# Kernel tuning notes

Hardware: AMD Instinct MI355X
Metric: run time of the kernel (lower is better)

Reference implementation:

```python
import jax, jax.numpy as jnp
import numpy as np
from jax import lax

NH = 4          # num_head
DIM = 512       # attention dim
VDIM = 512      # v_dim
QDIM = 1024     # q_dim
KS = 100        # loc_kernel_size -> conv width 2*KS+1
KN = 100        # loc_kernel_num
TEMP = 0.5      # temperature
BS, TS = 8, 2048


def setup_inputs() -> dict:
    key = jax.random.key(0)
    ks = jax.random.split(key, 12)
    s = 0.05
    return {
        "dec_state": jax.random.normal(ks[0], (BS, QDIM), jnp.float32),
        "enc_feat": jax.random.normal(ks[1], (BS, TS, VDIM), jnp.float32),
        "enc_len": jax.random.randint(ks[2], (BS,), TS // 2, TS + 1).astype(jnp.int32),
        "Wq": jax.random.normal(ks[3], (NH * DIM, QDIM), jnp.float32) * s,
        "bq": jnp.zeros((NH * DIM,), jnp.float32),
        "Wk": jax.random.normal(ks[4], (NH * DIM, VDIM), jnp.float32) * s,
        "bk": jnp.zeros((NH * DIM,), jnp.float32),
        "Wv": jax.random.normal(ks[5], (NH * VDIM, VDIM), jnp.float32) * s,
        "bv": jnp.zeros((NH * VDIM,), jnp.float32),
        "loc_conv_w": jax.random.normal(ks[6], (KN, NH, 2 * KS + 1), jnp.float32) * s,
        "loc_proj_w": jax.random.normal(ks[7], (DIM, KN), jnp.float32) * s,
        "gen_w": jax.random.normal(ks[8], (1, DIM), jnp.float32) * s,
        "gen_b": jnp.zeros((1,), jnp.float32),
        "merge_w": jax.random.normal(ks[9], (VDIM, NH * VDIM), jnp.float32) * s,
        "merge_b": jnp.zeros((VDIM,), jnp.float32),
    }


def reference(dec_state, enc_feat, enc_len, Wq, bq, Wk, bk, Wv, bv,
              loc_conv_w, loc_proj_w, gen_w, gen_b, merge_w, merge_b):
    bs, ts, _ = enc_feat.shape
    # query: [bs, nh, dim]
    query = jnp.tanh(dec_state @ Wq.T + bq).reshape(bs, NH, DIM)
    # key/value: [bs, nh, ts, dim]/[bs, nh, ts, v_dim]
    key = jnp.tanh(enc_feat @ Wk.T + bk).reshape(bs, ts, NH, DIM).transpose(0, 2, 1, 3)
    value = jnp.tanh(enc_feat @ Wv.T + bv).reshape(bs, ts, NH, VDIM).transpose(0, 2, 1, 3)
    # mask & initial (uniform-over-valid) previous attention
    pos = jnp.arange(ts)
    pad_mask = pos[None, :] >= enc_len[:, None]                      # [bs, ts] True = padded
    prev = jnp.where(pad_mask, 0.0, 1.0 / enc_len[:, None].astype(jnp.float32))  # [bs, ts]
    prev_att = jnp.broadcast_to(prev[:, None, :], (bs, NH, ts))      # [bs, nh, ts]
    # location features: Conv1d(nh -> kn, width 2*KS+1, pad KS, no bias)
    conv = lax.conv_general_dilated(prev_att, loc_conv_w, (1,), [(KS, KS)],
                                    dimension_numbers=("NCH", "OIH", "NCH"))  # [bs, kn, ts]
    loc = jnp.tanh(jnp.einsum("bkt,dk->btd", conv, loc_proj_w))      # [bs, ts, dim]
    # additive energy: gen_energy(tanh(k + q + loc))
    e = jnp.tanh(key + query[:, :, None, :] + loc[:, None, :, :])    # [bs, nh, ts, dim]
    energy = jnp.einsum("bhtd,d->bht", e, gen_w[0]) + gen_b[0]
    energy = energy / TEMP
    energy = jnp.where(pad_mask[:, None, :], -jnp.inf, energy)
    attn = jax.nn.softmax(energy, axis=-1)                           # [bs, nh, ts]
    ctx = jnp.einsum("bht,bhtv->bhv", attn, value).reshape(bs, NH * VDIM)
    context = ctx @ merge_w.T + merge_b                              # [bs, v_dim]
    return attn, context
```

## Files before the change

### kernel.cpp

```cpp
#include <hip/hip_runtime.h>
#include <math.h>

#define NH 4
#define DIM 512
#define VDIM 512
#define QDIM 1024
#define KS 100
#define KN 100
#define TEMPERATURE 0.5f
#define BS 8
#define TS 2048
#define NHD (NH * DIM)

#define WS_QUERY   0
#define WS_QTAB    16384
#define WS_ENERGYP 119808
#define WS_CTX     381952
#define WS_P       398336
#define WS_F32_END 418536

typedef __bf16 bf16x8 __attribute__((ext_vector_type(8)));
typedef __bf16 bf16x4 __attribute__((ext_vector_type(4)));
typedef _Float16 f16x8 __attribute__((ext_vector_type(8)));
typedef float  f32x4  __attribute__((ext_vector_type(4)));

#define AS1(p) ((const __attribute__((address_space(1))) void*)(p))
#define AS3(p) ((__attribute__((address_space(3))) void*)(p))

__device__ __forceinline__ float fast_tanh(float x) {
    float e = __expf(2.0f * x);
    return 1.0f - __fdividef(2.0f, e + 1.0f);
}

#define NE4 (BS * TS * VDIM / 4)
#define NW4 (NHD * VDIM / 4)
#define NCVT ((NE4 + 2 * NW4) / 256)
#define NQ2  (NHD / 4)
__global__ void k_pre(const float* __restrict__ enc, const float* __restrict__ Wk,
                      const float* __restrict__ Wv, __bf16* __restrict__ enc_bf,
                      __bf16* __restrict__ wk_bf, __bf16* __restrict__ wv_bf,
                      const float* __restrict__ dec, const float* __restrict__ Wq,
                      const float* __restrict__ bq, float* __restrict__ query,
                      const float* __restrict__ convw, float* __restrict__ P) {
    const int bx = blockIdx.x;
    if (bx < NCVT) {
        int i = bx * blockDim.x + threadIdx.x;
        const float* src; __bf16* dst; int k;
        if (i < NE4)            { src = enc; dst = enc_bf; k = i; }
        else if (i < NE4 + NW4) { src = Wk;  dst = wk_bf;  k = i - NE4; }
        else                    { src = Wv;  dst = wv_bf;  k = i - NE4 - NW4; }
        float4 v = ((const float4*)src)[k];
        bf16x4 o;
        o[0] = (__bf16)v.x; o[1] = (__bf16)v.y; o[2] = (__bf16)v.z; o[3] = (__bf16)v.w;
        ((bf16x4*)dst)[k] = o;
    } else if (bx < NCVT + NQ2) {
        int o = (bx - NCVT) * 4 + (threadIdx.x >> 6);
        int lane = threadIdx.x & 63;
        const float* wr = Wq + (size_t)o * QDIM;
        float s[BS];
        #pragma unroll
        for (int b = 0; b < BS; ++b) s[b] = 0.f;
        #pragma unroll
        for (int i = 0; i < QDIM / 64; ++i) {
            float wv = wr[lane + 64 * i];
            #pragma unroll
            for (int b = 0; b < BS; ++b)
                s[b] = fmaf(wv, dec[b * QDIM + lane + 64 * i], s[b]);
        }
        #pragma unroll
        for (int off = 32; off > 0; off >>= 1)
            #pragma unroll
            for (int b = 0; b < BS; ++b) s[b] += __shfl_down(s[b], off);
        if (lane == 0) {
            float bias = bq[o];
            #pragma unroll
            for (int b = 0; b < BS; ++b) query[b * NHD + o] = tanhf(s[b] + bias);
        }
    } else {
        __shared__ float cs[KN * (2 * KS + 1)];
        int tid = threadIdx.x;
        for (int i = tid; i < KN * (2 * KS + 1); i += 256) {
            int k = i / (2 * KS + 1);
            int dt = i - k * (2 * KS + 1);
            const float* wr = convw + k * (NH * (2 * KS + 1)) + dt;
            cs[i] = wr[0] + wr[201] + wr[402] + wr[603];
        }
        __syncthreads();
        if (tid < KN) {
            float acc = 0.f;
            P[tid] = 0.f;
            const float* c = cs + tid * (2 * KS + 1);
            for (int dt = 0; dt < 2 * KS + 1; ++dt) {
                acc += c[dt];
                P[(dt + 1) * KN + tid] = acc;
            }
        }
    }
}

__global__ void k_qtab(const float* __restrict__ P, const float* __restrict__ projw,
                       float* __restrict__ Qtab, float* __restrict__ ctx) {
    int tid = threadIdx.x;
    if (blockIdx.x >= 2 * KS + 2) {
        int z = (blockIdx.x - (2 * KS + 2)) * 512 + tid;
        ((float4*)ctx)[z] = make_float4(0.f, 0.f, 0.f, 0.f);
        return;
    }
    int j = blockIdx.x;
    __shared__ float Pc[KN];
    if (tid < KN) Pc[tid] = P[j * KN + tid];
    __syncthreads();
    const float* pr = projw + tid * KN;
    float s = 0.f;
    #pragma unroll 4
    for (int k = 0; k < KN; ++k) s = fmaf(pr[k], Pc[k], s);
    Qtab[j * DIM + tid] = s;
}

__global__ __launch_bounds__(512, 4) void k_fused(
    const __bf16* __restrict__ enc_bf, const __bf16* __restrict__ wk_bf,
    const __bf16* __restrict__ wv_bf, const float* __restrict__ bk,
    const float* __restrict__ bv, const float* __restrict__ gen_w,
    const int* __restrict__ enc_len, const float* __restrict__ query,
    const float* __restrict__ Qtab, float* __restrict__ energyP,
    _Float16* __restrict__ val) {
    const int bid = blockIdx.x;
    const int b   = bid >> 8;
    const int t0  = ((bid >> 4) & 15) << 7;
    const int n0  = ((((bid >> 3) & 1) << 3) | (bid & 7)) << 7;
    const int len = enc_len[b];
    if (t0 >= len) return;
    const int tid = threadIdx.x;
    const int w = tid >> 6, lane = tid & 63;
    const int wy = w >> 2, wx = w & 3;
    const int col = lane & 15, quad = lane >> 4;
    __shared__ __bf16 smem[3 * 12288];
    f32x4 accE[4][2], accV[4][2];
    #pragma unroll
    for (int i = 0; i < 4; ++i)
        #pragma unroll
        for (int j = 0; j < 2; ++j) { accE[i][j] = (f32x4)0.f; accV[i][j] = (f32x4)0.f; }
    const int sm = tid >> 2;
    const int sj = (tid & 3) ^ (sm & 3) ^ ((sm >> 2) & 3);
    const __bf16* gpA  = enc_bf + ((size_t)b * TS + t0) * VDIM + (size_t)sm * VDIM + sj * 8;
    const __bf16* gpBk = wk_bf + ((size_t)n0 + sm) * VDIM + sj * 8;
    const __bf16* gpBv = wv_bf + ((size_t)n0 + sm) * VDIM + sj * 8;
    const int cfr = quad ^ (col & 3) ^ ((col >> 2) & 3);
    const char* pbase = (const char*)smem;
    const int offA = (((wy * 64 + col) * 4 + cfr) << 4);
    const int offB = (((wx * 32 + col) * 4 + cfr) << 4);
    #define STG(sbe)                                                               \
        __builtin_amdgcn_global_load_lds(AS1(gpA),  AS3(smem + (sbe) + w * 512), 16, 0, 0);        \
        __builtin_amdgcn_global_load_lds(AS1(gpBk), AS3(smem + (sbe) + 4096 + w * 512), 16, 0, 0); \
        __builtin_amdgcn_global_load_lds(AS1(gpBv), AS3(smem + (sbe) + 8192 + w * 512), 16, 0, 0); \
        gpA += 32; gpBk += 32; gpBv += 32;
    STG(0)
    STG(12288)
    #pragma unroll
    for (int kk = 0; kk < 16; ++kk) {
        if (kk < 15)
            asm volatile("s_waitcnt vmcnt(3) lgkmcnt(0)\n\ts_barrier" ::: "memory");
        else
            asm volatile("s_waitcnt vmcnt(0) lgkmcnt(0)\n\ts_barrier" ::: "memory");
        if (kk < 14) {
            const int sbe = ((kk + 2) % 3) * 12288;
            STG(sbe)
        }
        const int bo = (kk % 3) * 24576;
        bf16x8 af[4], bfr[2];
        #pragma unroll
        for (int i = 0; i < 4; ++i) af[i] = *(const bf16x8*)(pbase + bo + offA + i * 1024);
        #pragma unroll
        for (int j = 0; j < 2; ++j) bfr[j] = *(const bf16x8*)(pbase + bo + 8192 + offB + j * 1024);
        #pragma unroll
        for (int i = 0; i < 4; ++i)
            #pragma unroll
            for (int j = 0; j < 2; ++j)
                accE[i][j] = __builtin_amdgcn_mfma_f32_16x16x32_bf16(af[i], bfr[j], accE[i][j], 0, 0, 0);
        #pragma unroll
        for (int j = 0; j < 2; ++j) bfr[j] = *(const bf16x8*)(pbase + bo + 16384 + offB + j * 1024);
        #pragma unroll
        for (int i = 0; i < 4; ++i)
            #pragma unroll
            for (int j = 0; j < 2; ++j)
                accV[i][j] = __builtin_amdgcn_mfma_f32_16x16x32_bf16(af[i], bfr[j], accV[i][j], 0, 0, 0);
    }
    #undef STG
    __syncthreads();

    _Float16* stage = (_Float16*)smem;
    float* red = (float*)((char*)smem + 32768);

    const int h = n0 >> 9;
    const float inv_len = 1.0f / (float)len;
    float qv[2], gw[2], bkv[2], bvv[2], lI[2];
    int dj[2];
    #pragma unroll
    for (int j = 0; j < 2; ++j) {
        int n = n0 + wx * 32 + j * 16 + col;
        dj[j] = n & (DIM - 1);
        qv[j] = query[b * NHD + n];
        gw[j] = gen_w[dj[j]];
        bkv[j] = bk[n];
        bvv[j] = bv[n];
        lI[j] = fast_tanh((Qtab[(2 * KS + 1) * DIM + dj[j]] - Qtab[dj[j]]) * inv_len);
    }
    #pragma unroll
    for (int i = 0; i < 4; ++i) {
        #pragma unroll
        for (int r = 0; r < 4; ++r) {
            int tl = wy * 64 + i * 16 + quad * 4 + r;
            int t = t0 + tl;
            float l[2];
            if (t >= KS && t < len - KS) {
                #pragma unroll
                for (int j = 0; j < 2; ++j) l[j] = lI[j];
            } else {
                int lo = KS - t; if (lo < 0) lo = 0;
                int hi = KS - t + len - 1; if (hi > 2 * KS) hi = 2 * KS;
                bool has = (hi >= lo);
                #pragma unroll
                for (int j = 0; j < 2; ++j) {
                    float cv = has
                        ? (Qtab[(hi + 1) * DIM + dj[j]] - Qtab[lo * DIM + dj[j]]) * inv_len
                        : 0.f;
                    l[j] = fast_tanh(cv);
                }
            }
            float s = 0.f;
            #pragma unroll
            for (int j = 0; j < 2; ++j) {
                float key = fast_tanh(accE[i][j][r] + bkv[j]);
                float e = fast_tanh(key + qv[j] + l[j]);
                s = fmaf(e, gw[j], s);
            }
            s += __shfl_xor(s, 1); s += __shfl_xor(s, 2);
            s += __shfl_xor(s, 4); s += __shfl_xor(s, 8);
            if (col == 0) red[tl * 4 + wx] = s;
        }
    }
    #pragma unroll
    for (int j = 0; j < 2; ++j) {
        #pragma unroll
        for (int i = 0; i < 4; ++i)
            #pragma unroll
            for (int r = 0; r < 4; ++r) {
                int tl = wy * 64 + i * 16 + quad * 4 + r;
                stage[tl * 128 + wx * 32 + j * 16 + col] =
                    (_Float16)fast_tanh(accV[i][j][r] + bvv[j]);
            }
    }
    __syncthreads();
    if (tid < 128) {
        float s = red[tid * 4] + red[tid * 4 + 1] + red[tid * 4 + 2] + red[tid * 4 + 3];
        energyP[(size_t)((n0 >> 7) & 3) * 65536 + (size_t)(b * NH + h) * TS + t0 + tid] = s;
    }
    #pragma unroll
    for (int it = 0; it < 4; ++it) {
        int idx = it * 512 + tid;
        int row = idx >> 4, seg = idx & 15;
        *(float4*)((char*)(val + ((size_t)b * TS + t0 + row) * NHD + n0) + seg * 16) =
            ((const float4*)stage)[idx];
    }
}

__global__ void k_softmax(const float* __restrict__ energyP, const int* __restrict__ enc_len,
                          const float* __restrict__ gen_b, float* __restrict__ attn) {
    int bh = blockIdx.x;
    int b = bh >> 2;
    int len = enc_len[b];
    int tid = threadIdx.x;
    int w = tid >> 6, lane = tid & 63;
    const float gb = gen_b[0];
    const float* e0 = energyP + (size_t)bh * TS;
    float ev[4];
    float mx = -INFINITY;
    #pragma unroll
    for (int i = 0; i < 4; ++i) {
        int t = i * 512 + tid;
        float e = -INFINITY;
        if (t < len) {
            float s = e0[t] + e0[65536 + t] + e0[131072 + t] + e0[196608 + t];
            e = (s + gb) * (1.0f / TEMPERATURE);
        }
        ev[i] = e;
        mx = fmaxf(mx, e);
    }
    __shared__ float sred[8], ssum[8];
    #pragma unroll
    for (int off = 32; off > 0; off >>= 1) mx = fmaxf(mx, __shfl_xor(mx, off));
    if (lane == 0) sred[w] = mx;
    __syncthreads();
    #pragma unroll
    for (int k = 0; k < 8; ++k) mx = fmaxf(mx, sred[k]);
    float ls = 0.f;
    #pragma unroll
    for (int i = 0; i < 4; ++i) {
        float ex = __expf(ev[i] - mx);
        ev[i] = ex;
        ls += ex;
    }
    #pragma unroll
    for (int off = 32; off > 0; off >>= 1) ls += __shfl_xor(ls, off);
    if (lane == 0) ssum[w] = ls;
    __syncthreads();
    float tot = 0.f;
    #pragma unroll
    for (int k = 0; k < 8; ++k) tot += ssum[k];
    float inv = 1.0f / tot;
    #pragma unroll
    for (int i = 0; i < 4; ++i)
        attn[(size_t)bh * TS + i * 512 + tid] = ev[i] * inv;
}

__global__ __launch_bounds__(256) void k_ctx2(const _Float16* __restrict__ val,
                                              const float* __restrict__ attn,
                                              const int* __restrict__ enc_len,
                                              float* __restrict__ ctx) {
    const int blk = blockIdx.x;
    const int b   = blk >> 7;
    const int nc  = (blk >> 3) & 15;
    const int tsl = blk & 7;
    const int len = enc_len[b];
    const int t0  = tsl * 256;
    if (t0 >= len) return;
    const int n0 = nc * 128;
    const int h  = n0 >> 9;
    const int tid = threadIdx.x;
    const int tn = tid & 15, tr = tid >> 4;
    const float* ar = attn + (size_t)(b * NH + h) * TS;
    float acc[8];
    #pragma unroll
    for (int k = 0; k < 8; ++k) acc[k] = 0.f;
    int tend = t0 + 256; if (tend > len) tend = len;
    for (int t = t0 + tr; t < tend; t += 16) {
        float a = ar[t];
        f16x8 v = *(const f16x8*)(val + ((size_t)b * TS + t) * NHD + n0 + tn * 8);
        #pragma unroll
        for (int k = 0; k < 8; ++k) acc[k] = fmaf(a, (float)v[k], acc[k]);
    }
    __shared__ float cred[16][128];
    #pragma unroll
    for (int k = 0; k < 8; ++k) cred[tr][tn * 8 + k] = acc[k];
    __syncthreads();
    if (tid < 128) {
        float s = 0.f;
        #pragma unroll
        for (int r = 0; r < 16; ++r) s += cred[r][tid];
        atomicAdd(&ctx[(size_t)b * NHD + n0 + tid], s);
    }
}

__global__ void k_merge(const float* __restrict__ ctx, const float* __restrict__ mw,
                        const float* __restrict__ mb, float* __restrict__ out) {
    int o = blockIdx.x * 4 + (threadIdx.x >> 6);
    int lane = threadIdx.x & 63;
    const float* wr = mw + (size_t)o * NHD;
    float s[BS];
    #pragma unroll
    for (int b = 0; b < BS; ++b) s[b] = 0.f;
    #pragma unroll
    for (int i = 0; i < NHD / 64; ++i) {
        float wv = wr[lane + 64 * i];
        #pragma unroll
        for (int b = 0; b < BS; ++b)
            s[b] = fmaf(wv, ctx[b * NHD + lane + 64 * i], s[b]);
    }
    #pragma unroll
    for (int off = 32; off > 0; off >>= 1)
        #pragma unroll
        for (int b = 0; b < BS; ++b) s[b] += __shfl_down(s[b], off);
    if (lane == 0) {
        float bias = mb[o];
        #pragma unroll
        for (int b = 0; b < BS; ++b) out[b * VDIM + o] = s[b] + bias;
    }
}

extern "C" void kernel_launch(void* const* d_in, const int* in_sizes, int n_in,
                              void* d_out, int out_size, void* d_ws, size_t ws_size,
                              hipStream_t stream) {
    const float* dec     = (const float*)d_in[0];
    const float* enc     = (const float*)d_in[1];
    const int*   enc_len = (const int*)d_in[2];
    const float* Wq      = (const float*)d_in[3];
    const float* bq      = (const float*)d_in[4];
    const float* Wk      = (const float*)d_in[5];
    const float* bk      = (const float*)d_in[6];
    const float* Wv      = (const float*)d_in[7];
    const float* bv      = (const float*)d_in[8];
    const float* convw   = (const float*)d_in[9];
    const float* projw   = (const float*)d_in[10];
    const float* gen_w   = (const float*)d_in[11];
    const float* gen_b   = (const float*)d_in[12];
    const float* merge_w = (const float*)d_in[13];
    const float* merge_b = (const float*)d_in[14];

    float* out    = (float*)d_out;
    float* ws     = (float*)d_ws;
    float* query  = ws + WS_QUERY;
    float* Qtab   = ws + WS_QTAB;
    float* energyP= ws + WS_ENERGYP;
    float* ctx    = ws + WS_CTX;
    float* Pws    = ws + WS_P;
    __bf16* enc_bf = (__bf16*)((char*)d_ws + (size_t)WS_F32_END * 4);
    __bf16* wk_bf  = enc_bf + (size_t)BS * TS * VDIM;
    __bf16* wv_bf  = wk_bf + (size_t)NHD * VDIM;
    _Float16* val  = (_Float16*)(wv_bf + (size_t)NHD * VDIM);

    k_pre<<<dim3(NCVT + NQ2 + 1), dim3(256), 0, stream>>>(
        enc, Wk, Wv, enc_bf, wk_bf, wv_bf, dec, Wq, bq, query, convw, Pws);
    k_qtab<<<dim3(2 * KS + 2 + 8), dim3(512), 0, stream>>>(Pws, projw, Qtab, ctx);
    k_fused<<<dim3(2048), dim3(512), 0, stream>>>(
        enc_bf, wk_bf, wv_bf, bk, bv, gen_w, enc_len, query, Qtab, energyP, val);
    k_softmax<<<dim3(BS * NH), dim3(512), 0, stream>>>(energyP, enc_len, gen_b, out);
    k_ctx2<<<dim3(BS * 16 * 8), dim3(256), 0, stream>>>(val, out, enc_len, ctx);
    k_merge<<<dim3(VDIM / 4), dim3(256), 0, stream>>>(ctx, merge_w, merge_b, out + 65536);
}
```

Baseline: 287.7 us.

## Enlarge fused GEMM tile to 256x128 with swizzled staging and MFMA priority

```diff
diff --git a/kernel.cpp b/kernel.cpp
--- a/kernel.cpp
+++ b/kernel.cpp
@@ -117,7 +117,7 @@
     Qtab[j * DIM + tid] = s;
 }
 
-__global__ __launch_bounds__(512, 4) void k_fused(
+__global__ __launch_bounds__(512, 2) void k_fused(
     const __bf16* __restrict__ enc_bf, const __bf16* __restrict__ wk_bf,
     const __bf16* __restrict__ wv_bf, const float* __restrict__ bk,
     const float* __restrict__ bv, const float* __restrict__ gen_w,
@@ -125,79 +125,86 @@
     const float* __restrict__ Qtab, float* __restrict__ energyP,
     _Float16* __restrict__ val) {
     const int bid = blockIdx.x;
-    const int b   = bid >> 8;
-    const int t0  = ((bid >> 4) & 15) << 7;
-    const int n0  = ((((bid >> 3) & 1) << 3) | (bid & 7)) << 7;
+    const int b   = bid >> 7;
+    const int t0  = ((bid >> 4) & 7) << 8;
+    const int nc  = (((bid >> 3) & 1) << 3) | (bid & 7);
+    const int n0  = nc << 7;
     const int len = enc_len[b];
     if (t0 >= len) return;
     const int tid = threadIdx.x;
     const int w = tid >> 6, lane = tid & 63;
-    const int wy = w >> 2, wx = w & 3;
+    const int wy = w >> 1, wx = w & 1;
     const int col = lane & 15, quad = lane >> 4;
-    __shared__ __bf16 smem[3 * 12288];
-    f32x4 accE[4][2], accV[4][2];
+    __shared__ __bf16 smem[3 * 16384];
+    f32x4 accE[4][4], accV[4][4];
     #pragma unroll
     for (int i = 0; i < 4; ++i)
         #pragma unroll
-        for (int j = 0; j < 2; ++j) { accE[i][j] = (f32x4)0.f; accV[i][j] = (f32x4)0.f; }
+        for (int j = 0; j < 4; ++j) { accE[i][j] = (f32x4)0.f; accV[i][j] = (f32x4)0.f; }
     const int sm = tid >> 2;
     const int sj = (tid & 3) ^ (sm & 3) ^ ((sm >> 2) & 3);
-    const __bf16* gpA  = enc_bf + ((size_t)b * TS + t0) * VDIM + (size_t)sm * VDIM + sj * 8;
+    const __bf16* gpA0 = enc_bf + ((size_t)b * TS + t0) * VDIM + (size_t)sm * VDIM + sj * 8;
+    const __bf16* gpA1 = gpA0 + (size_t)128 * VDIM;
     const __bf16* gpBk = wk_bf + ((size_t)n0 + sm) * VDIM + sj * 8;
     const __bf16* gpBv = wv_bf + ((size_t)n0 + sm) * VDIM + sj * 8;
     const int cfr = quad ^ (col & 3) ^ ((col >> 2) & 3);
     const char* pbase = (const char*)smem;
     const int offA = (((wy * 64 + col) * 4 + cfr) << 4);
-    const int offB = (((wx * 32 + col) * 4 + cfr) << 4);
-    #define STG(sbe)                                                               \
-        __builtin_amdgcn_global_load_lds(AS1(gpA),  AS3(smem + (sbe) + w * 512), 16, 0, 0);        \
-        __builtin_amdgcn_global_load_lds(AS1(gpBk), AS3(smem + (sbe) + 4096 + w * 512), 16, 0, 0); \
-        __builtin_amdgcn_global_load_lds(AS1(gpBv), AS3(smem + (sbe) + 8192 + w * 512), 16, 0, 0); \
-        gpA += 32; gpBk += 32; gpBv += 32;
+    const int offB = (((wx * 64 + col) * 4 + cfr) << 4);
+    #define STG(sbe)                                                                              \
+        __builtin_amdgcn_global_load_lds(AS1(gpA0), AS3(smem + (sbe) + w * 512), 16, 0, 0);        \
+        __builtin_amdgcn_global_load_lds(AS1(gpA1), AS3(smem + (sbe) + 4096 + w * 512), 16, 0, 0); \
+        __builtin_amdgcn_global_load_lds(AS1(gpBk), AS3(smem + (sbe) + 8192 + w * 512), 16, 0, 0); \
+        __builtin_amdgcn_global_load_lds(AS1(gpBv), AS3(smem + (sbe) + 12288 + w * 512), 16, 0, 0);\
+        gpA0 += 32; gpA1 += 32; gpBk += 32; gpBv += 32;
     STG(0)
-    STG(12288)
+    STG(16384)
     #pragma unroll
     for (int kk = 0; kk < 16; ++kk) {
         if (kk < 15)
-            asm volatile("s_waitcnt vmcnt(3) lgkmcnt(0)\n\ts_barrier" ::: "memory");
+            asm volatile("s_waitcnt vmcnt(4) lgkmcnt(0)\n\ts_barrier" ::: "memory");
         else
             asm volatile("s_waitcnt vmcnt(0) lgkmcnt(0)\n\ts_barrier" ::: "memory");
         if (kk < 14) {
-            const int sbe = ((kk + 2) % 3) * 12288;
+            const int sbe = ((kk + 2) % 3) * 16384;
             STG(sbe)
         }
-        const int bo = (kk % 3) * 24576;
-        bf16x8 af[4], bfr[2];
+        const int bo = (kk % 3) * 32768;
+        bf16x8 af[4], bfr[4];
         #pragma unroll
         for (int i = 0; i < 4; ++i) af[i] = *(const bf16x8*)(pbase + bo + offA + i * 1024);
         #pragma unroll
-        for (int j = 0; j < 2; ++j) bfr[j] = *(const bf16x8*)(pbase + bo + 8192 + offB + j * 1024);
+        for (int j = 0; j < 4; ++j) bfr[j] = *(const bf16x8*)(pbase + bo + 16384 + offB + j * 1024);
+        __builtin_amdgcn_s_setprio(1);
         #pragma unroll
         for (int i = 0; i < 4; ++i)
             #pragma unroll
-            for (int j = 0; j < 2; ++j)
+            for (int j = 0; j < 4; ++j)
                 accE[i][j] = __builtin_amdgcn_mfma_f32_16x16x32_bf16(af[i], bfr[j], accE[i][j], 0, 0, 0);
-        #pragma unroll
-        for (int j = 0; j < 2; ++j) bfr[j] = *(const bf16x8*)(pbase + bo + 16384 + offB + j * 1024);
+        __builtin_amdgcn_s_setprio(0);
+        #pragma unroll
+        for (int j = 0; j < 4; ++j) bfr[j] = *(const bf16x8*)(pbase + bo + 24576 + offB + j * 1024);
+        __builtin_amdgcn_s_setprio(1);
         #pragma unroll
         for (int i = 0; i < 4; ++i)
             #pragma unroll
-            for (int j = 0; j < 2; ++j)
+            for (int j = 0; j < 4; ++j)
                 accV[i][j] = __builtin_amdgcn_mfma_f32_16x16x32_bf16(af[i], bfr[j], accV[i][j], 0, 0, 0);
+        __builtin_amdgcn_s_setprio(0);
     }
     #undef STG
     __syncthreads();
 
     _Float16* stage = (_Float16*)smem;
-    float* red = (float*)((char*)smem + 32768);
-
-    const int h = n0 >> 9;
+    float* red = (float*)((char*)smem + 65536);
+
+    const int h = nc >> 2;
     const float inv_len = 1.0f / (float)len;
-    float qv[2], gw[2], bkv[2], bvv[2], lI[2];
-    int dj[2];
-    #pragma unroll
-    for (int j = 0; j < 2; ++j) {
-        int n = n0 + wx * 32 + j * 16 + col;
+    float qv[4], gw[4], bkv[4], bvv[4], lI[4];
+    int dj[4];
+    #pragma unroll
+    for (int j = 0; j < 4; ++j) {
+        int n = n0 + wx * 64 + j * 16 + col;
         dj[j] = n & (DIM - 1);
         qv[j] = query[b * NHD + n];
         gw[j] = gen_w[dj[j]];
@@ -211,16 +218,16 @@
         for (int r = 0; r < 4; ++r) {
             int tl = wy * 64 + i * 16 + quad * 4 + r;
             int t = t0 + tl;
-            float l[2];
+            float l[4];
             if (t >= KS && t < len - KS) {
                 #pragma unroll
-                for (int j = 0; j < 2; ++j) l[j] = lI[j];
+                for (int j = 0; j < 4; ++j) l[j] = lI[j];
             } else {
                 int lo = KS - t; if (lo < 0) lo = 0;
                 int hi = KS - t + len - 1; if (hi > 2 * KS) hi = 2 * KS;
                 bool has = (hi >= lo);
                 #pragma unroll
-                for (int j = 0; j < 2; ++j) {
+                for (int j = 0; j < 4; ++j) {
                     float cv = has
                         ? (Qtab[(hi + 1) * DIM + dj[j]] - Qtab[lo * DIM + dj[j]]) * inv_len
                         : 0.f;
@@ -229,38 +236,40 @@
             }
             float s = 0.f;
             #pragma unroll
-            for (int j = 0; j < 2; ++j) {
+            for (int j = 0; j < 4; ++j) {
                 float key = fast_tanh(accE[i][j][r] + bkv[j]);
                 float e = fast_tanh(key + qv[j] + l[j]);
                 s = fmaf(e, gw[j], s);
             }
             s += __shfl_xor(s, 1); s += __shfl_xor(s, 2);
             s += __shfl_xor(s, 4); s += __shfl_xor(s, 8);
-            if (col == 0) red[tl * 4 + wx] = s;
-        }
-    }
-    #pragma unroll
-    for (int j = 0; j < 2; ++j) {
+            if (col == 0) red[tl * 2 + wx] = s;
+        }
+    }
+    #pragma unroll
+    for (int j = 0; j < 4; ++j) {
         #pragma unroll
         for (int i = 0; i < 4; ++i)
             #pragma unroll
             for (int r = 0; r < 4; ++r) {
                 int tl = wy * 64 + i * 16 + quad * 4 + r;
-                stage[tl * 128 + wx * 32 + j * 16 + col] =
-                    (_Float16)fast_tanh(accV[i][j][r] + bvv[j]);
+                int nl = wx * 64 + j * 16 + col;
+                int snl = nl ^ (((tl >> 2) & 3) << 4);
+                stage[tl * 128 + snl] = (_Float16)fast_tanh(accV[i][j][r] + bvv[j]);
             }
     }
     __syncthreads();
-    if (tid < 128) {
-        float s = red[tid * 4] + red[tid * 4 + 1] + red[tid * 4 + 2] + red[tid * 4 + 3];
-        energyP[(size_t)((n0 >> 7) & 3) * 65536 + (size_t)(b * NH + h) * TS + t0 + tid] = s;
-    }
-    #pragma unroll
-    for (int it = 0; it < 4; ++it) {
+    if (tid < 256) {
+        float s = red[tid * 2] + red[tid * 2 + 1];
+        energyP[(size_t)(nc & 3) * 65536 + (size_t)(b * NH + h) * TS + t0 + tid] = s;
+    }
+    #pragma unroll
+    for (int it = 0; it < 8; ++it) {
         int idx = it * 512 + tid;
         int row = idx >> 4, seg = idx & 15;
-        *(float4*)((char*)(val + ((size_t)b * TS + t0 + row) * NHD + n0) + seg * 16) =
-            ((const float4*)stage)[idx];
+        int q = (row >> 2) & 3;
+        float4 vv = *(const float4*)((const char*)stage + row * 256 + ((seg * 16) ^ (q << 5)));
+        *(float4*)((char*)(val + ((size_t)b * TS + t0 + row) * NHD + n0) + seg * 16) = vv;
     }
 }
 
@@ -411,7 +420,7 @@
     k_pre<<<dim3(NCVT + NQ2 + 1), dim3(256), 0, stream>>>(
         enc, Wk, Wv, enc_bf, wk_bf, wv_bf, dec, Wq, bq, query, convw, Pws);
     k_qtab<<<dim3(2 * KS + 2 + 8), dim3(512), 0, stream>>>(Pws, projw, Qtab, ctx);
-    k_fused<<<dim3(2048), dim3(512), 0, stream>>>(
+    k_fused<<<dim3(1024), dim3(512), 0, stream>>>(
         enc_bf, wk_bf, wv_bf, bk, bv, gen_w, enc_len, query, Qtab, energyP, val);
     k_softmax<<<dim3(BS * NH), dim3(512), 0, stream>>>(energyP, enc_len, gen_b, out);
     k_ctx2<<<dim3(BS * 16 * 8), dim3(256), 0, stream>>>(val, out, enc_len, ctx);
```

Result: slower. 324.2 us (+12.7%).
